# Performance work log

Measured on AMD Instinct MI355X. Metric: run time of the kernel, lower is better.

## Reference

```python
import jax, jax.numpy as jnp
import numpy as np
from jax import lax

NUM_INITS = 64
MODEL_MODE = ['conv', 'conv', 'dense']
SIZE_ARRAY = [(16, 1, 5, 5), (16,), (32, 16, 5, 5), (32,), (10, 512), (10,)]
_flat = [int(np.prod(s)) for s in SIZE_ARRAY]
BP = np.concatenate(([0], np.cumsum(_flat)))  # breakpoints into flat param vector
TOTAL_PARAMS = int(BP[-1])  # 18378
BATCH_N = 128


def setup_inputs() -> dict:
    key = jax.random.key(0)
    k1, k2 = jax.random.split(key)
    params = jax.random.normal(k1, (NUM_INITS, TOTAL_PARAMS), dtype=jnp.float32) * 0.05
    batch = jax.random.normal(k2, (BATCH_N, 1, 28, 28), dtype=jnp.float32)
    return {"params": params, "batch": batch}


def _conv_relu_pool(x, w, b):
    # x: (N, C_in, H, W), w: (C_out, C_in, k, k), b: (C_out,)
    y = lax.conv_general_dilated(x, w, window_strides=(1, 1), padding='VALID',
                                 dimension_numbers=('NCHW', 'OIHW', 'NCHW'))
    y = jax.nn.relu(y + b[None, :, None, None])
    # MaxPool2d(2, 2) over spatial dims
    return lax.reduce_window(y, -jnp.inf, lax.max, (1, 1, 2, 2), (1, 1, 2, 2), 'VALID')


def reference(params, batch):
    # out: (num_inits, N, C, H, W) — ensemble replicated batch
    out = jnp.broadcast_to(batch[None], (NUM_INITS,) + batch.shape)
    i = 0
    for mode in MODEL_MODE:
        w = params[:, BP[i]:BP[i + 1]].reshape((NUM_INITS,) + SIZE_ARRAY[i])
        b = params[:, BP[i + 1]:BP[i + 2]].reshape((NUM_INITS,) + SIZE_ARRAY[i + 1])
        if mode == 'conv':
            # grouped conv over inits == vmap of dense conv over the init axis
            out = jax.vmap(_conv_relu_pool)(out, w, b)
        else:  # dense
            out = out.reshape(out.shape[0], out.shape[1], -1)  # flatten C,H,W
            out = jnp.einsum('inf,iof->ino', out, w) + b[:, None, :]
        i += 2
    return jax.nn.log_softmax(out, axis=2)  # (num_inits, N, 10)
```

## Files before the change

kernel.cpp:

```cpp
#include <hip/hip_runtime.h>
#include <hip/hip_bf16.h>
#include <math.h>

#define P_TOTAL 18378

typedef __attribute__((ext_vector_type(8))) short short8;
typedef __attribute__((ext_vector_type(4))) float float4v;
typedef __attribute__((ext_vector_type(16))) float float16;

__device__ __forceinline__ unsigned short f2bf(float f) {
    unsigned r;
    asm("v_cvt_pk_bf16_f32 %0, %1, %1" : "=v"(r) : "v"(f));
    return (unsigned short)r;
}

#define DPP_ADD_STEP(x, ctrl)                                                  \
    x += __int_as_float(__builtin_amdgcn_update_dpp(                           \
            0, __float_as_int(x), ctrl, 0xf, 0xf, true))

__device__ __forceinline__ float wave_reduce_sum63(float x) {
    DPP_ADD_STEP(x, 0x111);
    DPP_ADD_STEP(x, 0x112);
    DPP_ADD_STEP(x, 0x114);
    DPP_ADD_STEP(x, 0x118);
    DPP_ADD_STEP(x, 0x142);
    DPP_ADD_STEP(x, 0x143);
    return x;
}

__global__ __launch_bounds__(256) void prep_kernel(
        const float* __restrict__ params,
        const float* __restrict__ batch,
        unsigned short* __restrict__ wswz,
        float* __restrict__ w3lf,
        unsigned short* __restrict__ w1bf,
        unsigned short* __restrict__ Bmat) {
    int blk = blockIdx.x;
    int t = threadIdx.x;
    if (blk < 512) {
        int i = blk >> 3;
        int p = blk & 7;
        const float* P = params + (size_t)i * P_TOTAL;
        int s0 = p * 2304;
        for (int s = s0 + t; s < s0 + 2304; s += 256) {
            if (s < 12800) {
                int co = s / 400;
                int r = s - co * 400;
                int cin = r / 25;
                int sk = r - cin * 25;
                wswz[(size_t)i * 12800 + (sk * 32 + co) * 16 + cin] =
                    f2bf(P[416 + s]);
            } else if (s < 17920) {
                int k = s - 12800;
                int o = k >> 9, r = k & 511;
                int l = r >> 3, sl = r & 7;
                int co = l & 31, h = l >> 5;
                int py = sl >> 1, d = sl & 1;
                w3lf[(size_t)i * 5120 + k] =
                    P[13248 + o * 512 + co * 16 + py * 4 + 2 * h + d];
            } else {
                int e = s - 17920;
                int m = e >> 5, k = e & 31;
                w1bf[(size_t)i * 512 + e] =
                    (k < 25) ? f2bf(P[m * 25 + k]) : (unsigned short)0;
            }
        }
    } else {
        __shared__ float img[784];
        int jb = blk - 512;
        int j = jb >> 1;
        int half = jb & 1;
        const float* ip = batch + j * 784;
        for (int k = t; k < 784; k += 256) img[k] = ip[k];
        __syncthreads();
        unsigned short* dst = Bmat + (size_t)j * 18432;
        int task0 = half * 1152;
        for (int task = task0 + t; task < task0 + 1152; task += 256) {
            int c = task >> 2, kh = task & 3;
            int pp = c >> 2, q = c & 3;
            int py = pp / 12, px = pp - py * 12;
            int y0 = 2 * py + (q >> 1);
            int x0 = 2 * px + (q & 1);
            unsigned short ov[8] __attribute__((aligned(16)));
#pragma unroll
            for (int u = 0; u < 8; ++u) {
                int k = kh * 8 + u;
                float v = 0.f;
                if (k < 25) {
                    int ky = k / 5, kx = k - ky * 5;
                    v = img[(y0 + ky) * 28 + x0 + kx];
                }
                ov[u] = f2bf(v);
            }
            *(uint4*)(dst + c * 32 + kh * 8) = *(const uint4*)ov;
        }
    }
}

#define A1_PIX_STRIDE 24
#define IMG_LDS (144 * A1_PIX_STRIDE)
__global__ __launch_bounds__(256, 5) void mega_kernel(
        const float* __restrict__ params,
        const unsigned short* __restrict__ Bmat,
        const unsigned short* __restrict__ w1bf,
        const unsigned short* __restrict__ wswz,
        const float* __restrict__ w3lf,
        float* __restrict__ out) {
    __shared__ unsigned short a1s[4 * IMG_LDS];
    int b = blockIdx.x;
    int i = b & 63;
    int g = b >> 6;
    int t = threadIdx.x;
    int w = t >> 6;
    int lane = t & 63;
    int j = g * 4 + w;

    {
        int co = lane & 15;
        int h4 = lane >> 4;
        short8 wfr = *(const short8*)(w1bf + (size_t)i * 512 + co * 32 + h4 * 8);
        float bias1 = params[(size_t)i * P_TOTAL + 400 + co];
        unsigned short* dst = a1s + w * IMG_LDS;
        const unsigned short* bsrc = Bmat + (size_t)j * 18432;
#pragma unroll 6
        for (int nt = 0; nt < 36; ++nt) {
            short8 afr = *(const short8*)(bsrc + (nt * 16 + co) * 32 + h4 * 8);
            float4v acc = {0.f, 0.f, 0.f, 0.f};
            acc = __builtin_amdgcn_mfma_f32_16x16x32_bf16(afr, wfr, acc, 0, 0, 0);
            float v = fmaxf(fmaxf(acc[0], acc[1]), fmaxf(acc[2], acc[3]));
            v = fmaxf(v + bias1, 0.f);
            dst[(nt * 4 + h4) * A1_PIX_STRIDE + co] = f2bf(v);
        }
    }

    int n = lane & 31;
    int h = lane >> 5;
    const short8* wg = (const short8*)(wswz + (size_t)i * 12800 + n * 16 + h * 8);
    int y0 = n >> 3, x0 = n & 7;
    const unsigned short* bbase = a1s + w * IMG_LDS;
    const short8* pptr0 = (const short8*)(bbase + ((y0    ) * 12 + x0) * A1_PIX_STRIDE + h * 8);
    const short8* pptr1 = (const short8*)(bbase + ((y0 + 4) * 12 + x0) * A1_PIX_STRIDE + h * 8);

    float16 acc0 = {};
    float16 acc1 = {};
    __builtin_amdgcn_s_setprio(1);
#pragma unroll
    for (int ky = 0; ky < 5; ++ky) {
#pragma unroll
        for (int kx = 0; kx < 5; ++kx) {
            int tap = ky * 5 + kx;
            short8 wf = wg[tap * 64];
            int bo = (ky * 12 + kx) * 3;
            short8 p0 = pptr0[bo];
            short8 p1 = pptr1[bo];
            acc0 = __builtin_amdgcn_mfma_f32_32x32x16_bf16(p0, wf, acc0, 0, 0, 0);
            acc1 = __builtin_amdgcn_mfma_f32_32x32x16_bf16(p1, wf, acc1, 0, 0, 0);
        }
    }
    __builtin_amdgcn_s_setprio(0);

    int co2 = lane & 31;
    float bias2 = params[(size_t)i * P_TOTAL + 13216 + co2];
    float xr[8];
#pragma unroll
    for (int pyl = 0; pyl < 2; ++pyl) {
#pragma unroll
        for (int d = 0; d < 2; ++d) {
            int base = pyl * 8 + d * 2;
            float v0 = fmaxf(fmaxf(acc0[base], acc0[base + 1]),
                             fmaxf(acc0[base + 4], acc0[base + 5]));
            float v1 = fmaxf(fmaxf(acc1[base], acc1[base + 1]),
                             fmaxf(acc1[base + 4], acc1[base + 5]));
            xr[pyl * 2 + d]     = fmaxf(v0 + bias2, 0.f);
            xr[4 + pyl * 2 + d] = fmaxf(v1 + bias2, 0.f);
        }
    }

    const float* w3p = w3lf + (size_t)i * 5120 + lane * 8;
    float acc[10];
#pragma unroll
    for (int o = 0; o < 10; ++o) {
        float4v u0 = *(const float4v*)(w3p + o * 512);
        float4v u1 = *(const float4v*)(w3p + o * 512 + 4);
        float a = 0.f;
        a = fmaf(xr[0], u0[0], a);
        a = fmaf(xr[1], u0[1], a);
        a = fmaf(xr[2], u0[2], a);
        a = fmaf(xr[3], u0[3], a);
        a = fmaf(xr[4], u1[0], a);
        a = fmaf(xr[5], u1[1], a);
        a = fmaf(xr[6], u1[2], a);
        a = fmaf(xr[7], u1[3], a);
        acc[o] = wave_reduce_sum63(a);
    }
    if (lane == 63) {
        const float* bp = params + (size_t)i * P_TOTAL + 18368;
        float m = -3.4e38f;
#pragma unroll
        for (int o = 0; o < 10; ++o) { acc[o] += bp[o]; m = fmaxf(m, acc[o]); }
        float ssum = 0.f;
#pragma unroll
        for (int o = 0; o < 10; ++o) ssum += __expf(acc[o] - m);
        float ls = __logf(ssum) + m;
        float* op = out + ((size_t)i * 128 + j) * 10;
#pragma unroll
        for (int o = 0; o < 10; ++o) op[o] = acc[o] - ls;
    }
}

extern "C" void kernel_launch(void* const* d_in, const int* in_sizes, int n_in,
                              void* d_out, int out_size, void* d_ws, size_t ws_size,
                              hipStream_t stream) {
    const float* params = (const float*)d_in[0];
    const float* batch  = (const float*)d_in[1];
    float* out = (float*)d_out;

    unsigned short* wswz = (unsigned short*)d_ws;
    float* w3lf = (float*)((char*)d_ws + 1638400);
    unsigned short* w1bf = (unsigned short*)((char*)d_ws + 1638400 + 1310720);
    unsigned short* Bmat = (unsigned short*)((char*)d_ws + 1638400 + 1310720 + 65536);

    prep_kernel<<<768, 256, 0, stream>>>(params, batch, wswz, w3lf, w1bf, Bmat);
    mega_kernel<<<2048, 256, 0, stream>>>(params, Bmat, w1bf, wswz, w3lf, out);
}
```

Baseline: 97.50 us.

## Process two images per wave and XOR-swizzle conv1 activations in LDS

```diff
diff --git a/kernel.cpp b/kernel.cpp
--- a/kernel.cpp
+++ b/kernel.cpp
@@ -97,39 +97,50 @@
     }
 }
 
-#define A1_PIX_STRIDE 24
-#define IMG_LDS (144 * A1_PIX_STRIDE)
-__global__ __launch_bounds__(256, 5) void mega_kernel(
+#define A1_SLICE 2304
+__global__ __launch_bounds__(256, 4) void mega_kernel(
         const float* __restrict__ params,
         const unsigned short* __restrict__ Bmat,
         const unsigned short* __restrict__ w1bf,
         const unsigned short* __restrict__ wswz,
         const float* __restrict__ w3lf,
         float* __restrict__ out) {
-    __shared__ unsigned short a1s[4 * IMG_LDS];
+    __shared__ unsigned short a1s[8 * A1_SLICE];
     int b = blockIdx.x;
     int i = b & 63;
     int g = b >> 6;
     int t = threadIdx.x;
     int w = t >> 6;
     int lane = t & 63;
-    int j = g * 4 + w;
+    int j0 = g * 8 + w;
+    int j1 = j0 + 4;
+
+    unsigned short* s0 = a1s + w * (2 * A1_SLICE);
+    unsigned short* s1 = s0 + A1_SLICE;
 
     {
         int co = lane & 15;
         int h4 = lane >> 4;
         short8 wfr = *(const short8*)(w1bf + (size_t)i * 512 + co * 32 + h4 * 8);
         float bias1 = params[(size_t)i * P_TOTAL + 400 + co];
-        unsigned short* dst = a1s + w * IMG_LDS;
-        const unsigned short* bsrc = Bmat + (size_t)j * 18432;
-#pragma unroll 6
+        const unsigned short* ba = Bmat + (size_t)j0 * 18432;
+        const unsigned short* bb = Bmat + (size_t)j1 * 18432;
+        int ebase = h4 * 16 + co;
+#pragma unroll 4
         for (int nt = 0; nt < 36; ++nt) {
-            short8 afr = *(const short8*)(bsrc + (nt * 16 + co) * 32 + h4 * 8);
-            float4v acc = {0.f, 0.f, 0.f, 0.f};
-            acc = __builtin_amdgcn_mfma_f32_16x16x32_bf16(afr, wfr, acc, 0, 0, 0);
-            float v = fmaxf(fmaxf(acc[0], acc[1]), fmaxf(acc[2], acc[3]));
-            v = fmaxf(v + bias1, 0.f);
-            dst[(nt * 4 + h4) * A1_PIX_STRIDE + co] = f2bf(v);
+            short8 afr0 = *(const short8*)(ba + (nt * 16 + co) * 32 + h4 * 8);
+            short8 afr1 = *(const short8*)(bb + (nt * 16 + co) * 32 + h4 * 8);
+            float4v acca = {0.f, 0.f, 0.f, 0.f};
+            float4v accb = {0.f, 0.f, 0.f, 0.f};
+            acca = __builtin_amdgcn_mfma_f32_16x16x32_bf16(afr0, wfr, acca, 0, 0, 0);
+            accb = __builtin_amdgcn_mfma_f32_16x16x32_bf16(afr1, wfr, accb, 0, 0, 0);
+            float va = fmaxf(fmaxf(acca[0], acca[1]), fmaxf(acca[2], acca[3]));
+            float vb = fmaxf(fmaxf(accb[0], accb[1]), fmaxf(accb[2], accb[3]));
+            va = fmaxf(va + bias1, 0.f);
+            vb = fmaxf(vb + bias1, 0.f);
+            int e = (ebase + nt * 64) ^ ((nt & 7) << 3);
+            s0[e] = f2bf(va);
+            s1[e] = f2bf(vb);
         }
     }
 
@@ -137,12 +148,13 @@
     int h = lane >> 5;
     const short8* wg = (const short8*)(wswz + (size_t)i * 12800 + n * 16 + h * 8);
     int y0 = n >> 3, x0 = n & 7;
-    const unsigned short* bbase = a1s + w * IMG_LDS;
-    const short8* pptr0 = (const short8*)(bbase + ((y0    ) * 12 + x0) * A1_PIX_STRIDE + h * 8);
-    const short8* pptr1 = (const short8*)(bbase + ((y0 + 4) * 12 + x0) * A1_PIX_STRIDE + h * 8);
-
-    float16 acc0 = {};
-    float16 acc1 = {};
+    int pixbase = y0 * 12 + x0;
+    int h8 = h * 8;
+
+    float16 acc0a = {};
+    float16 acc1a = {};
+    float16 acc0b = {};
+    float16 acc1b = {};
     __builtin_amdgcn_s_setprio(1);
 #pragma unroll
     for (int ky = 0; ky < 5; ++ky) {
@@ -150,61 +162,86 @@
         for (int kx = 0; kx < 5; ++kx) {
             int tap = ky * 5 + kx;
             short8 wf = wg[tap * 64];
-            int bo = (ky * 12 + kx) * 3;
-            short8 p0 = pptr0[bo];
-            short8 p1 = pptr1[bo];
-            acc0 = __builtin_amdgcn_mfma_f32_32x32x16_bf16(p0, wf, acc0, 0, 0, 0);
-            acc1 = __builtin_amdgcn_mfma_f32_32x32x16_bf16(p1, wf, acc1, 0, 0, 0);
+            int plo = pixbase + ky * 12 + kx;
+            int phi = plo + 48;
+            int elo = (plo * 16 + h8) ^ (((plo >> 2) & 7) << 3);
+            int ehi = (phi * 16 + h8) ^ (((phi >> 2) & 7) << 3);
+            short8 p0a = *(const short8*)(s0 + elo);
+            short8 p1a = *(const short8*)(s0 + ehi);
+            short8 p0b = *(const short8*)(s1 + elo);
+            short8 p1b = *(const short8*)(s1 + ehi);
+            acc0a = __builtin_amdgcn_mfma_f32_32x32x16_bf16(p0a, wf, acc0a, 0, 0, 0);
+            acc1a = __builtin_amdgcn_mfma_f32_32x32x16_bf16(p1a, wf, acc1a, 0, 0, 0);
+            acc0b = __builtin_amdgcn_mfma_f32_32x32x16_bf16(p0b, wf, acc0b, 0, 0, 0);
+            acc1b = __builtin_amdgcn_mfma_f32_32x32x16_bf16(p1b, wf, acc1b, 0, 0, 0);
         }
     }
     __builtin_amdgcn_s_setprio(0);
 
     int co2 = lane & 31;
     float bias2 = params[(size_t)i * P_TOTAL + 13216 + co2];
-    float xr[8];
+    float xra[8], xrb[8];
 #pragma unroll
     for (int pyl = 0; pyl < 2; ++pyl) {
 #pragma unroll
         for (int d = 0; d < 2; ++d) {
             int base = pyl * 8 + d * 2;
-            float v0 = fmaxf(fmaxf(acc0[base], acc0[base + 1]),
-                             fmaxf(acc0[base + 4], acc0[base + 5]));
-            float v1 = fmaxf(fmaxf(acc1[base], acc1[base + 1]),
-                             fmaxf(acc1[base + 4], acc1[base + 5]));
-            xr[pyl * 2 + d]     = fmaxf(v0 + bias2, 0.f);
-            xr[4 + pyl * 2 + d] = fmaxf(v1 + bias2, 0.f);
+            float v0 = fmaxf(fmaxf(acc0a[base], acc0a[base + 1]),
+                             fmaxf(acc0a[base + 4], acc0a[base + 5]));
+            float v1 = fmaxf(fmaxf(acc1a[base], acc1a[base + 1]),
+                             fmaxf(acc1a[base + 4], acc1a[base + 5]));
+            xra[pyl * 2 + d]     = fmaxf(v0 + bias2, 0.f);
+            xra[4 + pyl * 2 + d] = fmaxf(v1 + bias2, 0.f);
+            v0 = fmaxf(fmaxf(acc0b[base], acc0b[base + 1]),
+                       fmaxf(acc0b[base + 4], acc0b[base + 5]));
+            v1 = fmaxf(fmaxf(acc1b[base], acc1b[base + 1]),
+                       fmaxf(acc1b[base + 4], acc1b[base + 5]));
+            xrb[pyl * 2 + d]     = fmaxf(v0 + bias2, 0.f);
+            xrb[4 + pyl * 2 + d] = fmaxf(v1 + bias2, 0.f);
         }
     }
 
     const float* w3p = w3lf + (size_t)i * 5120 + lane * 8;
-    float acc[10];
+    float aa[10], ab[10];
 #pragma unroll
     for (int o = 0; o < 10; ++o) {
         float4v u0 = *(const float4v*)(w3p + o * 512);
         float4v u1 = *(const float4v*)(w3p + o * 512 + 4);
-        float a = 0.f;
-        a = fmaf(xr[0], u0[0], a);
-        a = fmaf(xr[1], u0[1], a);
-        a = fmaf(xr[2], u0[2], a);
-        a = fmaf(xr[3], u0[3], a);
-        a = fmaf(xr[4], u1[0], a);
-        a = fmaf(xr[5], u1[1], a);
-        a = fmaf(xr[6], u1[2], a);
-        a = fmaf(xr[7], u1[3], a);
-        acc[o] = wave_reduce_sum63(a);
+        float ra = 0.f, rb = 0.f;
+        ra = fmaf(xra[0], u0[0], ra);  rb = fmaf(xrb[0], u0[0], rb);
+        ra = fmaf(xra[1], u0[1], ra);  rb = fmaf(xrb[1], u0[1], rb);
+        ra = fmaf(xra[2], u0[2], ra);  rb = fmaf(xrb[2], u0[2], rb);
+        ra = fmaf(xra[3], u0[3], ra);  rb = fmaf(xrb[3], u0[3], rb);
+        ra = fmaf(xra[4], u1[0], ra);  rb = fmaf(xrb[4], u1[0], rb);
+        ra = fmaf(xra[5], u1[1], ra);  rb = fmaf(xrb[5], u1[1], rb);
+        ra = fmaf(xra[6], u1[2], ra);  rb = fmaf(xrb[6], u1[2], rb);
+        ra = fmaf(xra[7], u1[3], ra);  rb = fmaf(xrb[7], u1[3], rb);
+        aa[o] = wave_reduce_sum63(ra);
+        ab[o] = wave_reduce_sum63(rb);
     }
     if (lane == 63) {
         const float* bp = params + (size_t)i * P_TOTAL + 18368;
         float m = -3.4e38f;
 #pragma unroll
-        for (int o = 0; o < 10; ++o) { acc[o] += bp[o]; m = fmaxf(m, acc[o]); }
+        for (int o = 0; o < 10; ++o) { aa[o] += bp[o]; m = fmaxf(m, aa[o]); }
         float ssum = 0.f;
 #pragma unroll
-        for (int o = 0; o < 10; ++o) ssum += __expf(acc[o] - m);
+        for (int o = 0; o < 10; ++o) ssum += __expf(aa[o] - m);
         float ls = __logf(ssum) + m;
-        float* op = out + ((size_t)i * 128 + j) * 10;
-#pragma unroll
-        for (int o = 0; o < 10; ++o) op[o] = acc[o] - ls;
+        float* op = out + ((size_t)i * 128 + j0) * 10;
+#pragma unroll
+        for (int o = 0; o < 10; ++o) op[o] = aa[o] - ls;
+
+        m = -3.4e38f;
+#pragma unroll
+        for (int o = 0; o < 10; ++o) { ab[o] += bp[o]; m = fmaxf(m, ab[o]); }
+        ssum = 0.f;
+#pragma unroll
+        for (int o = 0; o < 10; ++o) ssum += __expf(ab[o] - m);
+        ls = __logf(ssum) + m;
+        op = out + ((size_t)i * 128 + j1) * 10;
+#pragma unroll
+        for (int o = 0; o < 10; ++o) op[o] = ab[o] - ls;
     }
 }
 
@@ -221,5 +258,5 @@
     unsigned short* Bmat = (unsigned short*)((char*)d_ws + 1638400 + 1310720 + 65536);
 
     prep_kernel<<<768, 256, 0, stream>>>(params, batch, wswz, w3lf, w1bf, Bmat);
-    mega_kernel<<<2048, 256, 0, stream>>>(params, Bmat, w1bf, wswz, w3lf, out);
-}
+    mega_kernel<<<1024, 256, 0, stream>>>(params, Bmat, w1bf, wswz, w3lf, out);
+}
```

Result: faster. 92.21 us (-5.4%).
